# Optimization experiments

Measured on AMD Instinct MI355X. Metric: run time of the kernel, lower is better.

## Reference

```python
import jax, jax.numpy as jnp
import numpy as np

BS, DIM, N, M, O = 2048, 32, 40, 40, 200


def setup_inputs() -> dict:
    key = jax.random.key(0)
    k1, k2, k3 = jax.random.split(key, 3)
    x = jax.random.normal(k1, (BS, DIM, N), dtype=jnp.float32)
    y = jax.random.normal(k2, (BS, DIM, M), dtype=jnp.float32)
    # Linear(n*m -> o), no bias; scale like nn.Linear default-ish init
    W = jax.random.normal(k3, (O, N * M), dtype=jnp.float32) * (1.0 / np.sqrt(N * M))
    return {"x": x, "y": y, "W": W}


def reference(x, y, W):
    # Original math: z[b,d,n,m] = x[b,d,n] * y[b,d,m]; flatten (n,m) -> k; out = z @ W.T
    # Fused form: out[b,d,o] = sum_{n,m} x[b,d,n] * y[b,d,m] * W[o, n*M+m]
    o, nm = W.shape
    Wr = W.reshape(o, x.shape[-1], y.shape[-1])  # [O, N, M]
    return jnp.einsum('bdn,bdm,onm->bdo', x, y, Wr)
```

## Files before the change

kernel.cpp:

```cpp
#include <hip/hip_runtime.h>
#include <hip/hip_bf16.h>

#define BSZ   2048
#define DIMZ  32
#define NNv   40
#define MMv   40
#define OOv   200
#define KKv   1600
#define BD_TOTAL 65536
#define OPAD  208
#define NSTEPS 50
#define CHUNK_SLOTS 832
#define CHUNK_BYTES 13312
#define XPAD 44
#define YPAD 44

typedef __attribute__((ext_vector_type(8))) short short8;
typedef __attribute__((ext_vector_type(4))) float floatx4;

__global__ void wb_convert_kernel(const float* __restrict__ W,
                                  unsigned short* __restrict__ Wb) {
    int idx = blockIdx.x * 256 + threadIdx.x;
    if (idx >= NSTEPS * CHUNK_SLOTS * 8) return;
    int j    = idx & 7;
    int slot = (idx >> 3) % CHUNK_SLOTS;
    int c    = (idx >> 3) / CHUNK_SLOTS;
    int o    = slot >> 2;
    int kgs  = slot & 3;
    int kg   = kgs ^ ((o >> 1) & 3);
    int k    = c * 32 + kg * 8 + j;
    float v  = (o < OOv) ? W[o * KKv + k] : 0.0f;
    __hip_bfloat16 h = __float2bfloat16(v);
    Wb[idx] = *reinterpret_cast<unsigned short*>(&h);
}

__device__ __forceinline__ short f2bf(float f) {
    __hip_bfloat16 h = __float2bfloat16(f);
    return *reinterpret_cast<short*>(&h);
}

__device__ __forceinline__ void stageB(const unsigned short* __restrict__ Wb,
                                       int step, unsigned char* dst,
                                       int wave, int lane) {
    const char* src = (const char*)Wb + (size_t)step * CHUNK_BYTES;
    for (int c = wave; c < 13; c += 4) {
        int off = c * 1024 + lane * 16;
        __builtin_amdgcn_global_load_lds(
            (const __attribute__((address_space(1))) unsigned int*)(src + off),
            (__attribute__((address_space(3))) unsigned int*)(dst + off),
            16, 0, 0);
    }
}

__global__ __launch_bounds__(256, 2) void cin_mfma_kernel(
        const float* __restrict__ X, const float* __restrict__ Y,
        const unsigned short* __restrict__ Wb, float* __restrict__ Out) {
    __shared__ __align__(16) unsigned char smem[2 * CHUNK_BYTES + 128 * XPAD * 4 + 128 * YPAD * 4];
    unsigned char* bbuf0 = smem;
    unsigned char* bbuf1 = smem + CHUNK_BYTES;
    float* xlds = (float*)(smem + 2 * CHUNK_BYTES);
    float* ylds = (float*)(smem + 2 * CHUNK_BYTES + 128 * XPAD * 4);

    const int tid     = threadIdx.x;
    const int wave    = tid >> 6;
    const int lane    = tid & 63;
    const int li      = lane & 15;
    const int kg      = lane >> 4;
    const int rowhalf = wave & 1;
    const int colgrp  = wave >> 1;
    const int ntiles  = colgrp ? 6 : 7;
    const int obase   = colgrp * 112;
    const long blockbase = (long)blockIdx.x * 128;

    const float* xg = X + blockbase * NNv;
    const float* yg = Y + blockbase * MMv;
    for (int i = tid; i < 1280; i += 256) {
        int r  = i / 10;
        int c4 = (i % 10) * 4;
        floatx4 vx = *(const floatx4*)(xg + i * 4);
        *(floatx4*)(xlds + r * XPAD + c4) = vx;
        floatx4 vy = *(const floatx4*)(yg + i * 4);
        *(floatx4*)(ylds + r * YPAD + c4) = vy;
    }
    stageB(Wb, 0, bbuf0, wave, lane);
    __syncthreads();

    floatx4 acc[4][7];
#pragma unroll
    for (int rt = 0; rt < 4; ++rt)
#pragma unroll
        for (int ct = 0; ct < 7; ++ct)
            acc[rt][ct] = (floatx4){0.f, 0.f, 0.f, 0.f};

    int s = kg * 8;
    int n = 0;
    const int bfoff = (obase + li) * 64 + ((kg ^ ((li >> 1) & 3)) * 16);
    const int rowb  = rowhalf * 64 + li;

    for (int step = 0; step < NSTEPS; ++step) {
        unsigned char* cur = (step & 1) ? bbuf1 : bbuf0;
        unsigned char* nxt = (step & 1) ? bbuf0 : bbuf1;
        if (step + 1 < NSTEPS) stageB(Wb, step + 1, nxt, wave, lane);

        short8 bf[7];
#pragma unroll
        for (int ct = 0; ct < 7; ++ct)
            if (ct < ntiles)
                bf[ct] = *(const short8*)(cur + bfoff + ct * 1024);

        short8 af[4];
#pragma unroll
        for (int rt = 0; rt < 4; ++rt) {
            int row = rowb + rt * 16;
            float xv = xlds[row * XPAD + n];
            floatx4 y0 = *(const floatx4*)(ylds + row * YPAD + s);
            floatx4 y1 = *(const floatx4*)(ylds + row * YPAD + s + 4);
            short8 a;
            a[0] = f2bf(xv * y0.x); a[1] = f2bf(xv * y0.y);
            a[2] = f2bf(xv * y0.z); a[3] = f2bf(xv * y0.w);
            a[4] = f2bf(xv * y1.x); a[5] = f2bf(xv * y1.y);
            a[6] = f2bf(xv * y1.z); a[7] = f2bf(xv * y1.w);
            af[rt] = a;
        }

#pragma unroll
        for (int ct = 0; ct < 7; ++ct)
            if (ct < ntiles)
#pragma unroll
                for (int rt = 0; rt < 4; ++rt)
                    acc[rt][ct] = __builtin_amdgcn_mfma_f32_16x16x32_bf16(
                        af[rt], bf[ct], acc[rt][ct], 0, 0, 0);

        s += 32;
        if (s >= 40) { s -= 40; ++n; }
        __syncthreads();
    }

#pragma unroll
    for (int rt = 0; rt < 4; ++rt) {
#pragma unroll
        for (int ct = 0; ct < 7; ++ct) {
            if (ct >= ntiles) continue;
            int gcol = obase + ct * 16 + li;
            if (gcol < OOv) {
#pragma unroll
                for (int r4 = 0; r4 < 4; ++r4) {
                    long grow = blockbase + rowhalf * 64 + rt * 16 + kg * 4 + r4;
                    Out[grow * OOv + gcol] = acc[rt][ct][r4];
                }
            }
        }
    }
}

extern "C" void kernel_launch(void* const* d_in, const int* in_sizes, int n_in,
                              void* d_out, int out_size, void* d_ws, size_t ws_size,
                              hipStream_t stream) {
    (void)in_sizes; (void)n_in; (void)out_size; (void)ws_size;
    const float* X = (const float*)d_in[0];
    const float* Y = (const float*)d_in[1];
    const float* W = (const float*)d_in[2];
    float* Out = (float*)d_out;
    unsigned short* Wb = (unsigned short*)d_ws;

    wb_convert_kernel<<<1300, 256, 0, stream>>>(W, Wb);
    cin_mfma_kernel<<<512, 256, 0, stream>>>(X, Y, Wb, Out);
}
```

Before: 133.8 us.

## Load W fragments directly from global into registers, drop LDS staging and barriers

Removes the LDS double-buffer for the bf16 weight chunks. Each lane now loads its B fragments straight from global/L2 into registers, with the next step's fragments prefetched in a two-register ping-pong, and the per-step __syncthreads is eliminated. The weight layout drops the XOR swizzle because LDS bank conflicts no longer apply. The A-operand conversion also switches to packed two-float bf16 conversion. In exchange, register pressure rises (two sets of seven fragments), and every wave reloads weights from global memory instead of sharing them through LDS.

```diff
diff --git a/kernel.cpp b/kernel.cpp
--- a/kernel.cpp
+++ b/kernel.cpp
@@ -1,65 +1,46 @@
 #include <hip/hip_runtime.h>
 #include <hip/hip_bf16.h>
 
-#define BSZ   2048
-#define DIMZ  32
 #define NNv   40
 #define MMv   40
 #define OOv   200
 #define KKv   1600
-#define BD_TOTAL 65536
 #define OPAD  208
 #define NSTEPS 50
-#define CHUNK_SLOTS 832
 #define CHUNK_BYTES 13312
-#define XPAD 44
-#define YPAD 44
+#define PADR  44
 
 typedef __attribute__((ext_vector_type(8))) short short8;
 typedef __attribute__((ext_vector_type(4))) float floatx4;
+typedef __attribute__((ext_vector_type(4))) unsigned int uintx4;
 
 __global__ void wb_convert_kernel(const float* __restrict__ W,
                                   unsigned short* __restrict__ Wb) {
     int idx = blockIdx.x * 256 + threadIdx.x;
-    if (idx >= NSTEPS * CHUNK_SLOTS * 8) return;
+    if (idx >= NSTEPS * OPAD * 32) return;
     int j    = idx & 7;
-    int slot = (idx >> 3) % CHUNK_SLOTS;
-    int c    = (idx >> 3) / CHUNK_SLOTS;
+    int slot = (idx >> 3) % (OPAD * 4);
+    int c    = (idx >> 3) / (OPAD * 4);
     int o    = slot >> 2;
-    int kgs  = slot & 3;
-    int kg   = kgs ^ ((o >> 1) & 3);
+    int kg   = slot & 3;
     int k    = c * 32 + kg * 8 + j;
     float v  = (o < OOv) ? W[o * KKv + k] : 0.0f;
     __hip_bfloat16 h = __float2bfloat16(v);
     Wb[idx] = *reinterpret_cast<unsigned short*>(&h);
 }
 
-__device__ __forceinline__ short f2bf(float f) {
-    __hip_bfloat16 h = __float2bfloat16(f);
-    return *reinterpret_cast<short*>(&h);
-}
-
-__device__ __forceinline__ void stageB(const unsigned short* __restrict__ Wb,
-                                       int step, unsigned char* dst,
-                                       int wave, int lane) {
-    const char* src = (const char*)Wb + (size_t)step * CHUNK_BYTES;
-    for (int c = wave; c < 13; c += 4) {
-        int off = c * 1024 + lane * 16;
-        __builtin_amdgcn_global_load_lds(
-            (const __attribute__((address_space(1))) unsigned int*)(src + off),
-            (__attribute__((address_space(3))) unsigned int*)(dst + off),
-            16, 0, 0);
-    }
+__device__ __forceinline__ unsigned int cvt2(float a, float b) {
+    __hip_bfloat162 h = __float22bfloat162_rn(float2{a, b});
+    union { __hip_bfloat162 h2; unsigned int u; } cv;
+    cv.h2 = h;
+    return cv.u;
 }
 
 __global__ __launch_bounds__(256, 2) void cin_mfma_kernel(
         const float* __restrict__ X, const float* __restrict__ Y,
         const unsigned short* __restrict__ Wb, float* __restrict__ Out) {
-    __shared__ __align__(16) unsigned char smem[2 * CHUNK_BYTES + 128 * XPAD * 4 + 128 * YPAD * 4];
-    unsigned char* bbuf0 = smem;
-    unsigned char* bbuf1 = smem + CHUNK_BYTES;
-    float* xlds = (float*)(smem + 2 * CHUNK_BYTES);
-    float* ylds = (float*)(smem + 2 * CHUNK_BYTES + 128 * XPAD * 4);
+    __shared__ __align__(16) float xlds[128 * PADR];
+    __shared__ __align__(16) float ylds[128 * PADR];
 
     const int tid     = threadIdx.x;
     const int wave    = tid >> 6;
@@ -78,11 +59,10 @@
         int r  = i / 10;
         int c4 = (i % 10) * 4;
         floatx4 vx = *(const floatx4*)(xg + i * 4);
-        *(floatx4*)(xlds + r * XPAD + c4) = vx;
+        *(floatx4*)(xlds + r * PADR + c4) = vx;
         floatx4 vy = *(const floatx4*)(yg + i * 4);
-        *(floatx4*)(ylds + r * YPAD + c4) = vy;
+        *(floatx4*)(ylds + r * PADR + c4) = vy;
     }
-    stageB(Wb, 0, bbuf0, wave, lane);
     __syncthreads();
 
     floatx4 acc[4][7];
@@ -94,35 +74,30 @@
 
     int s = kg * 8;
     int n = 0;
-    const int bfoff = (obase + li) * 64 + ((kg ^ ((li >> 1) & 3)) * 16);
-    const int rowb  = rowhalf * 64 + li;
+    const int rowb = rowhalf * 64 + li;
 
-    for (int step = 0; step < NSTEPS; ++step) {
-        unsigned char* cur = (step & 1) ? bbuf1 : bbuf0;
-        unsigned char* nxt = (step & 1) ? bbuf0 : bbuf1;
-        if (step + 1 < NSTEPS) stageB(Wb, step + 1, nxt, wave, lane);
+    const char* bptr = (const char*)Wb + (obase + li) * 64 + kg * 16;
 
-        short8 bf[7];
+    short8 b0[7], b1[7];
 #pragma unroll
-        for (int ct = 0; ct < 7; ++ct)
-            if (ct < ntiles)
-                bf[ct] = *(const short8*)(cur + bfoff + ct * 1024);
+    for (int ct = 0; ct < 7; ++ct)
+        if (ct < ntiles) b0[ct] = *(const short8*)(bptr + ct * 1024);
 
+    auto compute = [&](short8 (&bf)[7]) {
         short8 af[4];
 #pragma unroll
         for (int rt = 0; rt < 4; ++rt) {
             int row = rowb + rt * 16;
-            float xv = xlds[row * XPAD + n];
-            floatx4 y0 = *(const floatx4*)(ylds + row * YPAD + s);
-            floatx4 y1 = *(const floatx4*)(ylds + row * YPAD + s + 4);
-            short8 a;
-            a[0] = f2bf(xv * y0.x); a[1] = f2bf(xv * y0.y);
-            a[2] = f2bf(xv * y0.z); a[3] = f2bf(xv * y0.w);
-            a[4] = f2bf(xv * y1.x); a[5] = f2bf(xv * y1.y);
-            a[6] = f2bf(xv * y1.z); a[7] = f2bf(xv * y1.w);
-            af[rt] = a;
+            float xv = xlds[row * PADR + n];
+            floatx4 y0 = *(const floatx4*)(ylds + row * PADR + s);
+            floatx4 y1 = *(const floatx4*)(ylds + row * PADR + s + 4);
+            union { short8 s8; uintx4 u4; } a;
+            a.u4[0] = cvt2(xv * y0.x, xv * y0.y);
+            a.u4[1] = cvt2(xv * y0.z, xv * y0.w);
+            a.u4[2] = cvt2(xv * y1.x, xv * y1.y);
+            a.u4[3] = cvt2(xv * y1.z, xv * y1.w);
+            af[rt] = a.s8;
         }
-
 #pragma unroll
         for (int ct = 0; ct < 7; ++ct)
             if (ct < ntiles)
@@ -130,10 +105,27 @@
                 for (int rt = 0; rt < 4; ++rt)
                     acc[rt][ct] = __builtin_amdgcn_mfma_f32_16x16x32_bf16(
                         af[rt], bf[ct], acc[rt][ct], 0, 0, 0);
-
         s += 32;
         if (s >= 40) { s -= 40; ++n; }
-        __syncthreads();
+    };
+
+#pragma unroll 1
+    for (int step = 0; step < NSTEPS; step += 2) {
+        if (step + 1 < NSTEPS) {
+#pragma unroll
+            for (int ct = 0; ct < 7; ++ct)
+                if (ct < ntiles)
+                    b1[ct] = *(const short8*)(bptr + CHUNK_BYTES + ct * 1024);
+        }
+        compute(b0);
+        if (step + 2 < NSTEPS) {
+#pragma unroll
+            for (int ct = 0; ct < 7; ++ct)
+                if (ct < ntiles)
+                    b0[ct] = *(const short8*)(bptr + 2 * CHUNK_BYTES + ct * 1024);
+        }
+        if (step + 1 < NSTEPS) compute(b1);
+        bptr += 2 * CHUNK_BYTES;
     }
 
 #pragma unroll
```

New measurement: 148.5 us. 11.0% more time.

## Switch to fp16 MFMA with packed A-fragment build and 64-row blocks

Applied to the files above, without the earlier changes.

Moves the GEMM from bf16 to fp16 MFMA. The A operand (x*y outer product) is now built with packed half-precision vector multiplies instead of per-element float multiply and bf16 conversion. Blocks shrink from 128 to 64 rows, so each of the four waves covers all rows with 3-4 column tiles, and the grid doubles to 1024 blocks with a launch bound of 3 blocks per CU. Y is stored in LDS as fp16 and x values are loaded once per group of 5 K-steps. This cuts VALU work per step and raises occupancy, but W chunks are staged twice as often per output row, and fp16 products of x*y carry a different rounding and overflow range than bf16.

```diff
diff --git a/kernel.cpp b/kernel.cpp
--- a/kernel.cpp
+++ b/kernel.cpp
@@ -1,48 +1,42 @@
 #include <hip/hip_runtime.h>
 #include <hip/hip_bf16.h>
+#include <hip/hip_fp16.h>
 
-#define BSZ   2048
-#define DIMZ  32
 #define NNv   40
 #define MMv   40
 #define OOv   200
 #define KKv   1600
-#define BD_TOTAL 65536
 #define OPAD  208
 #define NSTEPS 50
-#define CHUNK_SLOTS 832
 #define CHUNK_BYTES 13312
-#define XPAD 44
-#define YPAD 44
+#define XSTR  44
+#define YSTR  40
 
-typedef __attribute__((ext_vector_type(8))) short short8;
+typedef _Float16 half8  __attribute__((ext_vector_type(8)));
+typedef _Float16 half2v __attribute__((ext_vector_type(2)));
 typedef __attribute__((ext_vector_type(4))) float floatx4;
 
 __global__ void wb_convert_kernel(const float* __restrict__ W,
-                                  unsigned short* __restrict__ Wb) {
+                                  unsigned short* __restrict__ Wh) {
     int idx = blockIdx.x * 256 + threadIdx.x;
-    if (idx >= NSTEPS * CHUNK_SLOTS * 8) return;
+    if (idx >= NSTEPS * OPAD * 32) return;
     int j    = idx & 7;
-    int slot = (idx >> 3) % CHUNK_SLOTS;
-    int c    = (idx >> 3) / CHUNK_SLOTS;
+    int slot = (idx >> 3) % (OPAD * 4);
+    int c    = (idx >> 3) / (OPAD * 4);
     int o    = slot >> 2;
     int kgs  = slot & 3;
     int kg   = kgs ^ ((o >> 1) & 3);
     int k    = c * 32 + kg * 8 + j;
     float v  = (o < OOv) ? W[o * KKv + k] : 0.0f;
-    __hip_bfloat16 h = __float2bfloat16(v);
-    Wb[idx] = *reinterpret_cast<unsigned short*>(&h);
+    _Float16 h = (_Float16)v;
+    union { _Float16 h; unsigned short u; } cv; cv.h = h;
+    Wh[idx] = cv.u;
 }
 
-__device__ __forceinline__ short f2bf(float f) {
-    __hip_bfloat16 h = __float2bfloat16(f);
-    return *reinterpret_cast<short*>(&h);
-}
-
-__device__ __forceinline__ void stageB(const unsigned short* __restrict__ Wb,
+__device__ __forceinline__ void stageB(const unsigned short* __restrict__ Wh,
                                        int step, unsigned char* dst,
                                        int wave, int lane) {
-    const char* src = (const char*)Wb + (size_t)step * CHUNK_BYTES;
+    const char* src = (const char*)Wh + (size_t)step * CHUNK_BYTES;
     for (int c = wave; c < 13; c += 4) {
         int off = c * 1024 + lane * 16;
         __builtin_amdgcn_global_load_lds(
@@ -52,100 +46,118 @@
     }
 }
 
-__global__ __launch_bounds__(256, 2) void cin_mfma_kernel(
+__global__ __launch_bounds__(256, 3) void cin_mfma_kernel(
         const float* __restrict__ X, const float* __restrict__ Y,
-        const unsigned short* __restrict__ Wb, float* __restrict__ Out) {
-    __shared__ __align__(16) unsigned char smem[2 * CHUNK_BYTES + 128 * XPAD * 4 + 128 * YPAD * 4];
-    unsigned char* bbuf0 = smem;
-    unsigned char* bbuf1 = smem + CHUNK_BYTES;
-    float* xlds = (float*)(smem + 2 * CHUNK_BYTES);
-    float* ylds = (float*)(smem + 2 * CHUNK_BYTES + 128 * XPAD * 4);
+        const unsigned short* __restrict__ Wh, float* __restrict__ Out) {
+    __shared__ __align__(16) unsigned char bsm[2 * CHUNK_BYTES];
+    __shared__ __align__(16) float    xlds[64 * XSTR];
+    __shared__ __align__(16) _Float16 ylds[64 * YSTR];
 
-    const int tid     = threadIdx.x;
-    const int wave    = tid >> 6;
-    const int lane    = tid & 63;
-    const int li      = lane & 15;
-    const int kg      = lane >> 4;
-    const int rowhalf = wave & 1;
-    const int colgrp  = wave >> 1;
-    const int ntiles  = colgrp ? 6 : 7;
-    const int obase   = colgrp * 112;
-    const long blockbase = (long)blockIdx.x * 128;
+    const int tid  = threadIdx.x;
+    const int wave = tid >> 6;
+    const int lane = tid & 63;
+    const int li   = lane & 15;
+    const int kg   = lane >> 4;
+
+    static const int ctbase_t[4] = {0, 4, 7, 10};
+    const int cb      = ctbase_t[wave];
+    const int ntiles  = (wave == 0) ? 4 : 3;
+    const int obase   = cb * 16;
+    const long blockbase = (long)blockIdx.x * 64;
 
     const float* xg = X + blockbase * NNv;
     const float* yg = Y + blockbase * MMv;
-    for (int i = tid; i < 1280; i += 256) {
+    for (int i = tid; i < 640; i += 256) {
         int r  = i / 10;
         int c4 = (i % 10) * 4;
         floatx4 vx = *(const floatx4*)(xg + i * 4);
-        *(floatx4*)(xlds + r * XPAD + c4) = vx;
+        *(floatx4*)(xlds + r * XSTR + c4) = vx;
         floatx4 vy = *(const floatx4*)(yg + i * 4);
-        *(floatx4*)(ylds + r * YPAD + c4) = vy;
+        union { half2v h2[2]; unsigned long long u; } pk;
+        pk.h2[0] = (half2v){(_Float16)vy.x, (_Float16)vy.y};
+        pk.h2[1] = (half2v){(_Float16)vy.z, (_Float16)vy.w};
+        *(unsigned long long*)(ylds + r * YSTR + c4) = pk.u;
     }
-    stageB(Wb, 0, bbuf0, wave, lane);
+    stageB(Wh, 0, bsm, wave, lane);
     __syncthreads();
 
-    floatx4 acc[4][7];
+    floatx4 acc[4][4];
 #pragma unroll
     for (int rt = 0; rt < 4; ++rt)
 #pragma unroll
-        for (int ct = 0; ct < 7; ++ct)
+        for (int ct = 0; ct < 4; ++ct)
             acc[rt][ct] = (floatx4){0.f, 0.f, 0.f, 0.f};
 
-    int s = kg * 8;
-    int n = 0;
+    int soff[5];
+#pragma unroll
+    for (int j = 0; j < 5; ++j) soff[j] = (kg * 8 + 32 * j) % 40;
+
     const int bfoff = (obase + li) * 64 + ((kg ^ ((li >> 1) & 3)) * 16);
-    const int rowb  = rowhalf * 64 + li;
 
-    for (int step = 0; step < NSTEPS; ++step) {
-        unsigned char* cur = (step & 1) ? bbuf1 : bbuf0;
-        unsigned char* nxt = (step & 1) ? bbuf0 : bbuf1;
-        if (step + 1 < NSTEPS) stageB(Wb, step + 1, nxt, wave, lane);
+    for (int g = 0; g < 10; ++g) {
+        unsigned char* pA = bsm + ((g & 1) ? CHUNK_BYTES : 0);
+        unsigned char* pB = bsm + ((g & 1) ? 0 : CHUNK_BYTES);
+        const int n0 = g * 4;
 
-        short8 bf[7];
-#pragma unroll
-        for (int ct = 0; ct < 7; ++ct)
-            if (ct < ntiles)
-                bf[ct] = *(const short8*)(cur + bfoff + ct * 1024);
-
-        short8 af[4];
+        half2v xh[4][4];
 #pragma unroll
         for (int rt = 0; rt < 4; ++rt) {
-            int row = rowb + rt * 16;
-            float xv = xlds[row * XPAD + n];
-            floatx4 y0 = *(const floatx4*)(ylds + row * YPAD + s);
-            floatx4 y1 = *(const floatx4*)(ylds + row * YPAD + s + 4);
-            short8 a;
-            a[0] = f2bf(xv * y0.x); a[1] = f2bf(xv * y0.y);
-            a[2] = f2bf(xv * y0.z); a[3] = f2bf(xv * y0.w);
-            a[4] = f2bf(xv * y1.x); a[5] = f2bf(xv * y1.y);
-            a[6] = f2bf(xv * y1.z); a[7] = f2bf(xv * y1.w);
-            af[rt] = a;
+            floatx4 xq = *(const floatx4*)(xlds + (li + rt * 16) * XSTR + n0);
+            xh[rt][0] = (half2v){(_Float16)xq.x, (_Float16)xq.x};
+            xh[rt][1] = (half2v){(_Float16)xq.y, (_Float16)xq.y};
+            xh[rt][2] = (half2v){(_Float16)xq.z, (_Float16)xq.z};
+            xh[rt][3] = (half2v){(_Float16)xq.w, (_Float16)xq.w};
         }
 
 #pragma unroll
-        for (int ct = 0; ct < 7; ++ct)
-            if (ct < ntiles)
+        for (int j = 0; j < 5; ++j) {
+            const int step = g * 5 + j;
+            unsigned char* cur = (j & 1) ? pB : pA;
+            unsigned char* nxt = (j & 1) ? pA : pB;
+            if (step + 1 < NSTEPS) stageB(Wh, step + 1, nxt, wave, lane);
+
+            half8 bf[4];
 #pragma unroll
-                for (int rt = 0; rt < 4; ++rt)
-                    acc[rt][ct] = __builtin_amdgcn_mfma_f32_16x16x32_bf16(
-                        af[rt], bf[ct], acc[rt][ct], 0, 0, 0);
+            for (int ct = 0; ct < 4; ++ct)
+                if (ct < ntiles)
+                    bf[ct] = *(const half8*)(cur + bfoff + ct * 1024);
 
-        s += 32;
-        if (s >= 40) { s -= 40; ++n; }
-        __syncthreads();
+            half8 af[4];
+#pragma unroll
+            for (int rt = 0; rt < 4; ++rt) {
+                half2v xs;
+                if      (j == 0) xs = xh[rt][0];
+                else if (j == 1) xs = (kg == 0) ? xh[rt][0] : xh[rt][1];
+                else if (j == 2) xs = (kg < 2)  ? xh[rt][1] : xh[rt][2];
+                else if (j == 3) xs = (kg == 3) ? xh[rt][3] : xh[rt][2];
+                else             xs = xh[rt][3];
+                half8 xsp = __builtin_shufflevector(xs, xs, 0,1,0,1,0,1,0,1);
+                half8 yv = *(const half8*)(ylds + (li + rt * 16) * YSTR + soff[j]);
+                af[rt] = xsp * yv;
+            }
+
+#pragma unroll
+            for (int ct = 0; ct < 4; ++ct)
+                if (ct < ntiles)
+#pragma unroll
+                    for (int rt = 0; rt < 4; ++rt)
+                        acc[rt][ct] = __builtin_amdgcn_mfma_f32_16x16x32_f16(
+                            af[rt], bf[ct], acc[rt][ct], 0, 0, 0);
+
+            __syncthreads();
+        }
     }
 
 #pragma unroll
     for (int rt = 0; rt < 4; ++rt) {
 #pragma unroll
-        for (int ct = 0; ct < 7; ++ct) {
+        for (int ct = 0; ct < 4; ++ct) {
             if (ct >= ntiles) continue;
             int gcol = obase + ct * 16 + li;
             if (gcol < OOv) {
 #pragma unroll
                 for (int r4 = 0; r4 < 4; ++r4) {
-                    long grow = blockbase + rowhalf * 64 + rt * 16 + kg * 4 + r4;
+                    long grow = blockbase + rt * 16 + kg * 4 + r4;
                     Out[grow * OOv + gcol] = acc[rt][ct][r4];
                 }
             }
@@ -161,8 +173,8 @@
     const float* Y = (const float*)d_in[1];
     const float* W = (const float*)d_in[2];
     float* Out = (float*)d_out;
-    unsigned short* Wb = (unsigned short*)d_ws;
+    unsigned short* Wh = (unsigned short*)d_ws;
 
-    wb_convert_kernel<<<1300, 256, 0, stream>>>(W, Wb);
-    cin_mfma_kernel<<<512, 256, 0, stream>>>(X, Y, Wb, Out);
+    wb_convert_kernel<<<1300, 256, 0, stream>>>(W, Wh);
+    cin_mfma_kernel<<<1024, 256, 0, stream>>>(X, Y, Wh, Out);
 }
```

Result: slower. 150.2 us (+12.3%).
